# Optimization experiments

Hardware: AMD Instinct MI355X
Metric: run time of the kernel (lower is better)

Reference implementation:

```python
import jax, jax.numpy as jnp
import numpy as np

B, C, T, F = 4, 128, 512, 128
H, D = 4, 64              # n_head, hidden_channels
DV = C // H               # per-head value channels
EPS = 1e-5


def setup_inputs() -> dict:
    key = jax.random.key(0)
    ks = jax.random.split(key, 16)
    g = lambda k, s: jax.random.normal(k, s, dtype=jnp.float32) * 0.05
    inp = {
        'x': jax.random.normal(ks[0], (B, C, T, F), dtype=jnp.float32),
        # per-head Q/K/V 1x1 conv weights stacked over head axis
        'Wq': g(ks[1], (H, D, C)),  'bq': jnp.zeros((H, D), jnp.float32),
        'aq': jnp.full((H,), 0.25, jnp.float32),
        'lwq': jnp.ones((H, D, F), jnp.float32), 'lbq': jnp.zeros((H, D, F), jnp.float32),
        'Wk': g(ks[2], (H, D, C)),  'bk': jnp.zeros((H, D), jnp.float32),
        'ak': jnp.full((H,), 0.25, jnp.float32),
        'lwk': jnp.ones((H, D, F), jnp.float32), 'lbk': jnp.zeros((H, D, F), jnp.float32),
        'Wv': g(ks[3], (H, DV, C)), 'bv': jnp.zeros((H, DV), jnp.float32),
        'av': jnp.full((H,), 0.25, jnp.float32),
        'lwv': jnp.ones((H, DV, F), jnp.float32), 'lbv': jnp.zeros((H, DV, F), jnp.float32),
        # after_attention: 1x1 conv C->C + PReLU(scalar) + TLN([C, F])
        'Wo': g(ks[4], (C, C)), 'bo': jnp.zeros((C,), jnp.float32),
        'ao': jnp.float32(0.25),
        'lwo': jnp.ones((C, F), jnp.float32), 'lbo': jnp.zeros((C, F), jnp.float32),
    }
    return inp


def _proj(x, W, b, a, lw, lb):
    """1x1 conv (per head) + PReLU + LayerNorm over (channel, freq). x:[B,C,T,F] -> [B,H,D,T,F]."""
    y = jnp.einsum('bctf,hdc->bhdtf', x, W) + b[None, :, :, None, None]
    y = jnp.where(y >= 0, y, a[None, :, None, None, None] * y)
    mu = jnp.mean(y, axis=(2, 4), keepdims=True)
    var = jnp.mean(jnp.square(y - mu), axis=(2, 4), keepdims=True)
    y = (y - mu) * jax.lax.rsqrt(var + EPS)
    return y * lw[None, :, :, None, :] + lb[None, :, :, None, :]


def reference(x, Wq, bq, aq, lwq, lbq, Wk, bk, ak, lwk, lbk,
              Wv, bv, av, lwv, lbv, Wo, bo, ao, lwo, lbo):
    Bx, Cx, Tx, Fx = x.shape
    q = _proj(x, Wq, bq, aq, lwq, lbq)   # [B,H,D,T,F]
    k = _proj(x, Wk, bk, ak, lwk, lbk)   # [B,H,D,T,F]
    v = _proj(x, Wv, bv, av, lwv, lbv)   # [B,H,DV,T,F]
    # flatten as torch: transpose(1,2) then reshape -> feature layout (channel, freq)
    qf = q.transpose(0, 1, 3, 2, 4).reshape(Bx, H, Tx, D * Fx)
    kf = k.transpose(0, 1, 3, 2, 4).reshape(Bx, H, Tx, D * Fx)
    vf = v.transpose(0, 1, 3, 2, 4).reshape(Bx, H, Tx, DV * Fx)
    scale = 1.0 / jnp.sqrt(jnp.float32(Fx * D))
    attn = jax.nn.softmax(jnp.einsum('bhtd,bhsd->bhts', qf, kf) * scale, axis=-1)
    out = jnp.einsum('bhts,bhsd->bhtd', attn, vf)          # [B,H,T,DV*F]
    # concat heads (head-major) -> [B,T,C,F] -> [B,C,T,F]
    r = out.transpose(0, 2, 1, 3).reshape(Bx, Tx, Cx, Fx).transpose(0, 2, 1, 3)
    z = jnp.einsum('bctf,dc->bdtf', r, Wo) + bo[None, :, None, None]
    z = jnp.where(z >= 0, z, ao * z)
    mu = jnp.mean(z, axis=(1, 3), keepdims=True)
    var = jnp.mean(jnp.square(z - mu), axis=(1, 3), keepdims=True)
    z = (z - mu) * jax.lax.rsqrt(var + EPS)
    z = z * lwo[None, :, None, :] + lbo[None, :, None, :]
    return z + x
```

## Files before the change

kernel.cpp:

```cpp
#include <hip/hip_runtime.h>
#include <hip/hip_bf16.h>

constexpr int B = 4, C = 128, T = 512, F = 128, H = 4, D = 64, DV = 32;
constexpr int E  = D * F;
constexpr int EV = DV * F;
constexpr float EPS = 1e-5f;


typedef __attribute__((ext_vector_type(4))) float f32x4;
typedef __attribute__((ext_vector_type(8))) short bf16x8;

__device__ __forceinline__ float bf2f(unsigned short u) {
  return __uint_as_float(((unsigned int)u) << 16);
}
__device__ __forceinline__ unsigned short f2bf(float f) {
  unsigned int b = __float_as_uint(f);
  unsigned int r = b + 0x7FFFu + ((b >> 16) & 1u);
  return (unsigned short)(r >> 16);
}

__device__ __forceinline__ void gl_lds16(const unsigned short* g, unsigned short* l) {
  __builtin_amdgcn_global_load_lds(
      (const __attribute__((address_space(1))) unsigned int*)(g),
      (__attribute__((address_space(3))) unsigned int*)(l), 16, 0, 0);
}

__global__ __launch_bounds__(256) void prep_kernel(
    const float* __restrict__ Wq, const float* __restrict__ Wk,
    const float* __restrict__ Wv, const float* __restrict__ Wo,
    const float* __restrict__ bq, const float* __restrict__ bk,
    const float* __restrict__ bv, const float* __restrict__ aq,
    const float* __restrict__ ak, const float* __restrict__ av,
    const float* __restrict__ lwq, const float* __restrict__ lwk,
    const float* __restrict__ lwv, const float* __restrict__ lbq,
    const float* __restrict__ lbk, const float* __restrict__ lbv,
    unsigned short* __restrict__ Wall, unsigned short* __restrict__ Wo2,
    float* __restrict__ ball, float* __restrict__ aall,
    float* __restrict__ lwall, float* __restrict__ lball,
    float* __restrict__ lwI, float* __restrict__ lbI) {
  int i = blockIdx.x * 256 + threadIdx.x;
  if (i < 81920) {
    float w = (i < 32768) ? Wq[i] : (i < 65536) ? Wk[i - 32768] : Wv[i - 65536];
    Wall[i] = f2bf(w);
    float lw = (i < 32768) ? lwq[i] : (i < 65536) ? lwk[i - 32768] : lwv[i - 65536];
    float lb = (i < 32768) ? lbq[i] : (i < 65536) ? lbk[i - 32768] : lbv[i - 65536];
    lwall[i] = lw;
    lball[i] = lb;
    int gm = i >> 7, f = i & 127;
    if (gm >= 512) {
      int hm = gm - 512;
      size_t idx = ((size_t)(hm >> 2) * 128 + f) * 4 + (hm & 3);
      lwI[idx] = lw;
      lbI[idx] = lb;
    }
  }
  if (i < 16384) Wo2[i] = f2bf(Wo[i]);
  if (i < 640) {
    ball[i] = (i < 256) ? bq[i] : (i < 512) ? bk[i - 256] : bv[i - 512];
    aall[i] = (i < 256) ? aq[i >> 6] : (i < 512) ? ak[(i - 256) >> 6] : av[(i - 512) >> 5];
  }
}

__global__ __launch_bounds__(256) void xT_kernel(const float* __restrict__ x,
                                                 unsigned short* __restrict__ xT) {
  __shared__ unsigned short tile[128][136];
  int bx = blockIdx.x;
  int t = bx & 511;
  int b = bx >> 9;
  int tid = threadIdx.x;
#pragma unroll
  for (int j = 0; j < 16; ++j) {
    int ch = j * 256 + tid;
    int c = ch >> 5;
    int fc = ch & 31;
    float4 v = *reinterpret_cast<const float4*>(
        x + (((size_t)b * C + c) * T + t) * F + fc * 4);
    unsigned short o[4] = {f2bf(v.x), f2bf(v.y), f2bf(v.z), f2bf(v.w)};
    *reinterpret_cast<ushort4*>(&tile[c][fc * 4]) = *reinterpret_cast<const ushort4*>(o);
  }
  __syncthreads();
  int f = tid >> 1, half = tid & 1;
  unsigned short* dst = xT + ((size_t)b * 65536 + (size_t)t * 128 + f) * 128 + half * 64;
#pragma unroll
  for (int g8 = 0; g8 < 8; ++g8) {
    unsigned short o[8];
#pragma unroll
    for (int kk = 0; kk < 8; ++kk) o[kk] = tile[half * 64 + g8 * 8 + kk][f];
    *reinterpret_cast<uint4*>(dst + g8 * 8) = *reinterpret_cast<const uint4*>(o);
  }
}

__global__ __launch_bounds__(256) void proj_gemm_kernel(
    const unsigned short* __restrict__ Wall, const unsigned short* __restrict__ xT,
    const float* __restrict__ ball, const float* __restrict__ aall,
    const float* __restrict__ lwall, const float* __restrict__ lball,
    const float* __restrict__ lwI, const float* __restrict__ lbI,
    unsigned short* __restrict__ qf, unsigned short* __restrict__ kf,
    unsigned short* __restrict__ vf) {
  __shared__ alignas(16) unsigned short As[128 * 64];
  __shared__ alignas(16) unsigned short Bs[128 * 64];
  __shared__ float part[4][2][2];

  int p = blockIdx.x;
  int cpx = gridDim.x >> 3;
  int v = (p & 7) * cpx + (p >> 3);
  int bb = v / 2560;
  int tl = v - bb * 2560;
  int tm = tl / 512;
  int t = tl - tm * 512;

  int tid = threadIdx.x;
  int w = tid >> 6, lane = tid & 63;
  int wr = w >> 1, wc = w & 1;
  int lr = lane & 15, kg = lane >> 4;

  const unsigned short* Ab = Wall + (size_t)tm * 128 * 128;
  const unsigned short* Bb = xT + ((size_t)bb * 65536 + (size_t)t * 128) * 128;

  f32x4 acc[4][4] = {};
  for (int k0 = 0; k0 < 128; k0 += 64) {
#pragma unroll
    for (int j = 0; j < 4; ++j) {
      int ch = j * 256 + tid;
      int r = ch >> 3;
      int c = (ch & 7) * 8;
      gl_lds16(Ab + (size_t)r * 128 + k0 + c, &As[ch * 8]);
      gl_lds16(Bb + (size_t)r * 128 + k0 + c, &Bs[ch * 8]);
    }
    __syncthreads();
#pragma unroll
    for (int ks = 0; ks < 2; ++ks) {
      bf16x8 af[4], bfr[4];
#pragma unroll
      for (int m = 0; m < 4; ++m)
        af[m] = *reinterpret_cast<const bf16x8*>(
            &As[(wr * 64 + m * 16 + lr) * 64 + ks * 32 + kg * 8]);
#pragma unroll
      for (int n = 0; n < 4; ++n)
        bfr[n] = *reinterpret_cast<const bf16x8*>(
            &Bs[(wc * 64 + n * 16 + lr) * 64 + ks * 32 + kg * 8]);
#pragma unroll
      for (int m = 0; m < 4; ++m)
#pragma unroll
        for (int n = 0; n < 4; ++n)
          acc[m][n] = __builtin_amdgcn_mfma_f32_16x16x32_bf16(af[m], bfr[n], acc[m][n], 0, 0, 0);
    }
    __syncthreads();
  }

  int sec = (tm < 2) ? 0 : (tm < 4 ? 1 : 2);
  float s[2] = {0.f, 0.f}, s2[2] = {0.f, 0.f};
#pragma unroll
  for (int m = 0; m < 4; ++m) {
    int g = (sec == 2) ? (m >> 1) : 0;
    int gm0 = tm * 128 + wr * 64 + m * 16 + kg * 4;
    float4 bi4 = *reinterpret_cast<const float4*>(&ball[gm0]);
    float4 al4 = *reinterpret_cast<const float4*>(&aall[gm0]);
    const float bi[4] = {bi4.x, bi4.y, bi4.z, bi4.w};
    const float al[4] = {al4.x, al4.y, al4.z, al4.w};
#pragma unroll
    for (int j = 0; j < 4; ++j) {
#pragma unroll
      for (int n = 0; n < 4; ++n) {
        float val = acc[m][n][j] + bi[j];
        val = val >= 0.f ? val : al[j] * val;
        acc[m][n][j] = val;
        s[g] += val;
        s2[g] += val * val;
      }
    }
  }
#pragma unroll
  for (int off = 32; off >= 1; off >>= 1) {
    s[0] += __shfl_xor(s[0], off, 64);
    s2[0] += __shfl_xor(s2[0], off, 64);
    s[1] += __shfl_xor(s[1], off, 64);
    s2[1] += __shfl_xor(s2[1], off, 64);
  }
  if (lane == 0) {
    part[w][0][0] = s[0]; part[w][0][1] = s2[0];
    part[w][1][0] = s[1]; part[w][1][1] = s2[1];
  }
  __syncthreads();
  float invN = (sec == 2) ? (1.f / 4096.f) : (1.f / 8192.f);
  float mu[2], rs[2];
#pragma unroll
  for (int g = 0; g < 2; ++g) {
    float S = part[2 * wr][g][0] + part[2 * wr + 1][g][0];
    float S2 = part[2 * wr][g][1] + part[2 * wr + 1][g][1];
    float m_ = S * invN;
    float var = S2 * invN - m_ * m_;
    mu[g] = m_;
    rs[g] = rsqrtf(var + EPS);
  }

#pragma unroll
  for (int m = 0; m < 4; ++m) {
    int g = (sec == 2) ? (m >> 1) : 0;
    float mu_ = mu[g], rs_ = rs[g];
    int row0 = wr * 64 + m * 16 + kg * 4;
    int gm0 = tm * 128 + row0;
    if (sec < 2) {
#pragma unroll
      for (int j = 0; j < 4; ++j) {
        int gm = gm0 + j;
        const float* lwr = lwall + (size_t)gm * 128;
        const float* lbr = lball + (size_t)gm * 128;
        unsigned short* dst;
        if (sec == 0) {
          int h = gm >> 6, d = gm & 63;
          dst = qf + (((size_t)bb * H + h) * T + t) * E + d * 128;
        } else {
          int hm = gm - 256, h = hm >> 6, d = hm & 63;
          dst = kf + (((size_t)bb * H + h) * T + t) * E + d * 128;
        }
#pragma unroll
        for (int n = 0; n < 4; ++n) {
          int f = wc * 64 + n * 16 + lr;
          dst[f] = f2bf((acc[m][n][j] - mu_) * rs_ * lwr[f] + lbr[f]);
        }
      }
    } else {
      int hm = gm0 - 512;
      int h = hm >> 5, d0 = hm & 31;
      int gmg = hm >> 2;
      unsigned short* dstb = vf + (((size_t)bb * H + h) * T + t) * EV;
      const float* lw0 = lwI + (size_t)gmg * 512;
      const float* lb0 = lbI + (size_t)gmg * 512;
#pragma unroll
      for (int n = 0; n < 4; ++n) {
        int f = wc * 64 + n * 16 + lr;
        float4 w4 = *reinterpret_cast<const float4*>(lw0 + f * 4);
        float4 b4 = *reinterpret_cast<const float4*>(lb0 + f * 4);
        unsigned short o[4];
        o[0] = f2bf((acc[m][n][0] - mu_) * rs_ * w4.x + b4.x);
        o[1] = f2bf((acc[m][n][1] - mu_) * rs_ * w4.y + b4.y);
        o[2] = f2bf((acc[m][n][2] - mu_) * rs_ * w4.z + b4.z);
        o[3] = f2bf((acc[m][n][3] - mu_) * rs_ * w4.w + b4.w);
        *reinterpret_cast<ushort4*>(dstb + (size_t)f * 32 + d0) =
            *reinterpret_cast<const ushort4*>(o);
      }
    }
  }
}

template <bool OUT_BF16>
__global__ __launch_bounds__(256) void gemm_bt_kernel(
    const unsigned short* __restrict__ A, const unsigned short* __restrict__ Bm,
    void* __restrict__ Out, int M, int N, int K, float scale,
    int tiles_m, int tiles_n, int kchunks, int nb) {
  __shared__ alignas(16) unsigned short As[128 * 64];
  __shared__ alignas(16) unsigned short Bs[128 * 64];

  int p = blockIdx.x;
  int cpx = gridDim.x >> 3;
  int v = (p & 7) * cpx + (p >> 3);
  int tpb = tiles_m * tiles_n;
  int per_bh = tpb * kchunks;
  int bh = v / per_bh;
  int r0 = v - bh * per_bh;
  int kc = r0 / tpb;
  int tl = r0 - kc * tpb;
  int tm = tl / tiles_n;
  int tn = tl - tm * tiles_n;

  int tid = threadIdx.x;
  int w = tid >> 6, lane = tid & 63;
  int wr = w >> 1, wc = w & 1;
  int lr = lane & 15, kg = lane >> 4;

  const unsigned short* Ab = A + ((size_t)bh * M + tm * 128) * K;
  const unsigned short* Bb = Bm + ((size_t)bh * N + tn * 128) * K;

  int klen = K / kchunks;
  int kb = kc * klen;

  f32x4 acc[4][4] = {};
  for (int k0 = kb; k0 < kb + klen; k0 += 64) {
#pragma unroll
    for (int j = 0; j < 4; ++j) {
      int ch = j * 256 + tid;
      int r = ch >> 3;
      int c = (ch & 7) * 8;
      gl_lds16(Ab + (size_t)r * K + k0 + c, &As[ch * 8]);
      gl_lds16(Bb + (size_t)r * K + k0 + c, &Bs[ch * 8]);
    }
    __syncthreads();
#pragma unroll
    for (int ks = 0; ks < 2; ++ks) {
      bf16x8 af[4], bf[4];
#pragma unroll
      for (int m = 0; m < 4; ++m)
        af[m] = *reinterpret_cast<const bf16x8*>(
            &As[(wr * 64 + m * 16 + lr) * 64 + ks * 32 + kg * 8]);
#pragma unroll
      for (int n = 0; n < 4; ++n)
        bf[n] = *reinterpret_cast<const bf16x8*>(
            &Bs[(wc * 64 + n * 16 + lr) * 64 + ks * 32 + kg * 8]);
#pragma unroll
      for (int m = 0; m < 4; ++m)
#pragma unroll
        for (int n = 0; n < 4; ++n)
          acc[m][n] = __builtin_amdgcn_mfma_f32_16x16x32_bf16(af[m], bf[n], acc[m][n], 0, 0, 0);
    }
    __syncthreads();
  }

  int orow = tm * 128 + wr * 64 + kg * 4;
  int ocol = tn * 128 + wc * 64 + lr;
  size_t obase = (size_t)(kc * nb + bh) * M * N;
  if constexpr (OUT_BF16) {
    unsigned short* O = (unsigned short*)Out + obase;
#pragma unroll
    for (int m = 0; m < 4; ++m)
#pragma unroll
      for (int j = 0; j < 4; ++j) {
        size_t base = (size_t)(orow + m * 16 + j) * N + ocol;
#pragma unroll
        for (int n = 0; n < 4; ++n)
          O[base + n * 16] = f2bf(acc[m][n][j] * scale);
      }
  } else {
    float* O = (float*)Out + obase;
#pragma unroll
    for (int m = 0; m < 4; ++m)
#pragma unroll
      for (int j = 0; j < 4; ++j) {
        size_t base = (size_t)(orow + m * 16 + j) * N + ocol;
#pragma unroll
        for (int n = 0; n < 4; ++n)
          O[base + n * 16] = acc[m][n][j] * scale;
      }
  }
}

__global__ __launch_bounds__(256) void transpose_v_kernel(
    const unsigned short* __restrict__ src, unsigned short* __restrict__ dst) {
  __shared__ unsigned short tile[64][72];
  int bx = blockIdx.x;
  int et = bx & 63;
  int tt = (bx >> 6) & 7;
  int bh = bx >> 9;
  const unsigned short* sb = src + ((size_t)bh * T + tt * 64) * EV + et * 64;
#pragma unroll
  for (int j = 0; j < 2; ++j) {
    int ch = j * 256 + threadIdx.x;
    int r = ch >> 3;
    int c8 = ch & 7;
    uint4 u = *reinterpret_cast<const uint4*>(sb + (size_t)r * EV + c8 * 8);
    *reinterpret_cast<uint4*>(&tile[r][c8 * 8]) = u;
  }
  __syncthreads();
  unsigned short* db = dst + ((size_t)bh * EV + et * 64) * T + tt * 64;
#pragma unroll
  for (int j = 0; j < 2; ++j) {
    int ch = j * 256 + threadIdx.x;
    int r = ch >> 3;
    int c8 = ch & 7;
    unsigned short o[8];
#pragma unroll
    for (int i = 0; i < 8; ++i) o[i] = tile[c8 * 8 + i][r];
    *reinterpret_cast<uint4*>(db + (size_t)r * T + c8 * 8) =
        *reinterpret_cast<const uint4*>(o);
  }
}

__global__ __launch_bounds__(64) void softmax_kernel(const float* __restrict__ a,
                                                     unsigned short* __restrict__ ob,
                                                     int nchunk) {
  const size_t cs = (size_t)8192 * 512;
  const float* pr = a + (size_t)blockIdx.x * T;
  int tid = threadIdx.x;
  float4 v0 = *reinterpret_cast<const float4*>(pr + tid * 8);
  float4 v1 = *reinterpret_cast<const float4*>(pr + tid * 8 + 4);
  for (int c = 1; c < nchunk; ++c) {
    float4 u0 = *reinterpret_cast<const float4*>(pr + c * cs + tid * 8);
    float4 u1 = *reinterpret_cast<const float4*>(pr + c * cs + tid * 8 + 4);
    v0.x += u0.x; v0.y += u0.y; v0.z += u0.z; v0.w += u0.w;
    v1.x += u1.x; v1.y += u1.y; v1.z += u1.z; v1.w += u1.w;
  }
  float mx = fmaxf(fmaxf(fmaxf(v0.x, v0.y), fmaxf(v0.z, v0.w)),
                   fmaxf(fmaxf(v1.x, v1.y), fmaxf(v1.z, v1.w)));
#pragma unroll
  for (int off = 32; off >= 1; off >>= 1) mx = fmaxf(mx, __shfl_xor(mx, off, 64));
  v0.x = __expf(v0.x - mx); v0.y = __expf(v0.y - mx);
  v0.z = __expf(v0.z - mx); v0.w = __expf(v0.w - mx);
  v1.x = __expf(v1.x - mx); v1.y = __expf(v1.y - mx);
  v1.z = __expf(v1.z - mx); v1.w = __expf(v1.w - mx);
  float sm = v0.x + v0.y + v0.z + v0.w + v1.x + v1.y + v1.z + v1.w;
#pragma unroll
  for (int off = 32; off >= 1; off >>= 1) sm += __shfl_xor(sm, off, 64);
  float r = 1.0f / sm;
  uint4 o;
  o.x = (unsigned int)f2bf(v0.x * r) | ((unsigned int)f2bf(v0.y * r) << 16);
  o.y = (unsigned int)f2bf(v0.z * r) | ((unsigned int)f2bf(v0.w * r) << 16);
  o.z = (unsigned int)f2bf(v1.x * r) | ((unsigned int)f2bf(v1.y * r) << 16);
  o.w = (unsigned int)f2bf(v1.z * r) | ((unsigned int)f2bf(v1.w * r) << 16);
  *reinterpret_cast<uint4*>(ob + (size_t)blockIdx.x * T + tid * 8) = o;
}

__global__ __launch_bounds__(256) void outproj_gemm_kernel(
    const unsigned short* __restrict__ Wo2, const unsigned short* __restrict__ pv,
    const float* __restrict__ bo, const float* __restrict__ ao,
    const float* __restrict__ lwo, const float* __restrict__ lbo,
    const float* __restrict__ x, float* __restrict__ outp) {
  __shared__ alignas(16) unsigned short As[128 * 64];
  __shared__ alignas(16) unsigned short Bs[128 * 64];
  __shared__ float part[4][2];

  int p = blockIdx.x;
  int cpx = gridDim.x >> 3;
  int v = (p & 7) * cpx + (p >> 3);
  int bb = v >> 9;
  int t = v & 511;

  int tid = threadIdx.x;
  int w = tid >> 6, lane = tid & 63;
  int wr = w >> 1, wc = w & 1;
  int lr = lane & 15, kg = lane >> 4;

  const unsigned short* pvb = pv + (size_t)bb * H * T * EV + (size_t)t * EV;

  f32x4 acc[4][4] = {};
  for (int k0 = 0; k0 < 128; k0 += 64) {
#pragma unroll
    for (int j = 0; j < 4; ++j) {
      int ch = j * 256 + tid;
      int r = ch >> 3;
      int c0 = (ch & 7) * 8;
      gl_lds16(Wo2 + (size_t)r * 128 + k0 + c0, &As[ch * 8]);
      int cc = k0 + c0;
      int h = cc >> 5, dv0 = cc & 31;
      gl_lds16(pvb + (size_t)h * T * EV + (size_t)r * 32 + dv0, &Bs[ch * 8]);
    }
    __syncthreads();
#pragma unroll
    for (int ks = 0; ks < 2; ++ks) {
      bf16x8 af[4], bf[4];
#pragma unroll
      for (int m = 0; m < 4; ++m)
        af[m] = *reinterpret_cast<const bf16x8*>(
            &As[(wr * 64 + m * 16 + lr) * 64 + ks * 32 + kg * 8]);
#pragma unroll
      for (int n = 0; n < 4; ++n)
        bf[n] = *reinterpret_cast<const bf16x8*>(
            &Bs[(wc * 64 + n * 16 + lr) * 64 + ks * 32 + kg * 8]);
#pragma unroll
      for (int m = 0; m < 4; ++m)
#pragma unroll
        for (int n = 0; n < 4; ++n)
          acc[m][n] = __builtin_amdgcn_mfma_f32_16x16x32_bf16(af[m], bf[n], acc[m][n], 0, 0, 0);
    }
    __syncthreads();
  }

  float aO = ao[0];
  float s = 0.f, s2 = 0.f;
#pragma unroll
  for (int m = 0; m < 4; ++m)
#pragma unroll
    for (int j = 0; j < 4; ++j) {
      int d = wr * 64 + m * 16 + kg * 4 + j;
      float bi = bo[d];
#pragma unroll
      for (int n = 0; n < 4; ++n) {
        float val = acc[m][n][j] + bi;
        val = val >= 0.f ? val : aO * val;
        acc[m][n][j] = val;
        s += val;
        s2 += val * val;
      }
    }
#pragma unroll
  for (int off = 32; off >= 1; off >>= 1) {
    s += __shfl_xor(s, off, 64);
    s2 += __shfl_xor(s2, off, 64);
  }
  if (lane == 0) { part[w][0] = s; part[w][1] = s2; }
  __syncthreads();
  float S = part[0][0] + part[1][0] + part[2][0] + part[3][0];
  float S2 = part[0][1] + part[1][1] + part[2][1] + part[3][1];
  const float invN = 1.f / 16384.f;
  float mu = S * invN;
  float var = S2 * invN - mu * mu;
  float rstd = rsqrtf(var + EPS);
#pragma unroll
  for (int m = 0; m < 4; ++m)
#pragma unroll
    for (int j = 0; j < 4; ++j) {
      int d = wr * 64 + m * 16 + kg * 4 + j;
#pragma unroll
      for (int n = 0; n < 4; ++n) {
        int f = wc * 64 + n * 16 + lr;
        float val = (acc[m][n][j] - mu) * rstd * lwo[d * 128 + f] + lbo[d * 128 + f];
        size_t xi = (((size_t)bb * C + d) * T + t) * F + f;
        outp[xi] = val + x[xi];
      }
    }
}

extern "C" void kernel_launch(void* const* d_in, const int* in_sizes, int n_in,
                              void* d_out, int out_size, void* d_ws, size_t ws_size,
                              hipStream_t stream) {
  const float* x   = (const float*)d_in[0];
  const float* Wq  = (const float*)d_in[1];
  const float* bq  = (const float*)d_in[2];
  const float* aq  = (const float*)d_in[3];
  const float* lwq = (const float*)d_in[4];
  const float* lbq = (const float*)d_in[5];
  const float* Wk  = (const float*)d_in[6];
  const float* bk_ = (const float*)d_in[7];
  const float* ak  = (const float*)d_in[8];
  const float* lwk = (const float*)d_in[9];
  const float* lbk = (const float*)d_in[10];
  const float* Wv  = (const float*)d_in[11];
  const float* bv  = (const float*)d_in[12];
  const float* av  = (const float*)d_in[13];
  const float* lwv = (const float*)d_in[14];
  const float* lbv = (const float*)d_in[15];
  const float* Wo  = (const float*)d_in[16];
  const float* bo  = (const float*)d_in[17];
  const float* ao  = (const float*)d_in[18];
  const float* lwo = (const float*)d_in[19];
  const float* lbo = (const float*)d_in[20];
  float* outp = (float*)d_out;

  char* ws = (char*)d_ws;
  unsigned short* qfp = (unsigned short*)(ws);
  unsigned short* kfp = (unsigned short*)(ws + 134217728ull);
  unsigned short* vfp = (unsigned short*)(ws + 268435456ull);
  unsigned short* xT  = (unsigned short*)(ws + 335544320ull);
  float*          atnP = (float*)(ws + 335544320ull);
  unsigned short* Wall = (unsigned short*)(ws + 402653184ull);
  unsigned short* Wo2  = (unsigned short*)(ws + 402849792ull);
  float*          lwall = (float*)(ws + 402915328ull);
  float*          lball = (float*)(ws + 403243008ull);
  float*          ball = (float*)(ws + 403570688ull);
  float*          aall = (float*)(ws + 403574784ull);
  float*          lwI  = (float*)(ws + 403578880ull);
  float*          lbI  = (float*)(ws + 403644416ull);
  unsigned short* atnb = (unsigned short*)(ws);
  unsigned short* vfT  = (unsigned short*)(ws + 134217728ull);
  unsigned short* pvp  = (unsigned short*)(ws + 268435456ull);

  prep_kernel<<<320, 256, 0, stream>>>(Wq, Wk, Wv, Wo, bq, bk_, bv, aq, ak, av,
                                       lwq, lwk, lwv, lbq, lbk, lbv,
                                       Wall, Wo2, ball, aall, lwall, lball,
                                       lwI, lbI);

  xT_kernel<<<2048, 256, 0, stream>>>(x, xT);

  proj_gemm_kernel<<<10240, 256, 0, stream>>>(Wall, xT, ball, aall,
                                              lwall, lball, lwI, lbI,
                                              qfp, kfp, vfp);

  gemm_bt_kernel<false><<<1024, 256, 0, stream>>>(
      qfp, kfp, atnP, 512, 512, 8192, 0.011048543456039806f, 4, 4, 4, 16);

  transpose_v_kernel<<<8192, 256, 0, stream>>>(vfp, vfT);

  softmax_kernel<<<8192, 64, 0, stream>>>(atnP, atnb, 4);

  gemm_bt_kernel<true><<<2048, 256, 0, stream>>>(
      atnb, vfT, pvp, 512, 4096, 512, 1.0f, 4, 32, 1, 16);

  outproj_gemm_kernel<<<2048, 256, 0, stream>>>(Wo2, pvp, bo, ao, lwo, lbo, x, outp);
}
```

Baseline: 546.6 us.

## Store QK^T split-K partials in fp16, halve split count, reuse bf16 xT residual

The QK^T GEMM now uses 2 K-chunks instead of 4 and writes its partial scores as fp16 instead of fp32. The softmax kernel reads and sums these fp16 partials, which cuts the bytes written and read for the score partials. The output projection now takes its residual from the bf16 transposed copy xT, prefetched into LDS with a swizzle, instead of reading fp32 x from global memory. The risks are lower precision in the scores and in the residual add (bf16 x added to the output), fewer QK blocks for parallelism, and workspace offsets that were reshuffled so the partials fit in a new region.

```diff
diff --git a/kernel.cpp b/kernel.cpp
--- a/kernel.cpp
+++ b/kernel.cpp
@@ -1,5 +1,6 @@
 #include <hip/hip_runtime.h>
 #include <hip/hip_bf16.h>
+#include <hip/hip_fp16.h>
 
 constexpr int B = 4, C = 128, T = 512, F = 128, H = 4, D = 64, DV = 32;
 constexpr int E  = D * F;
@@ -17,6 +18,13 @@
   unsigned int b = __float_as_uint(f);
   unsigned int r = b + 0x7FFFu + ((b >> 16) & 1u);
   return (unsigned short)(r >> 16);
+}
+__device__ __forceinline__ unsigned short f2h(float f) {
+  __half h = __float2half(f);
+  return __half_as_ushort(h);
+}
+__device__ __forceinline__ float h2f(unsigned short u) {
+  return __half2float(__ushort_as_half(u));
 }
 
 __device__ __forceinline__ void gl_lds16(const unsigned short* g, unsigned short* l) {
@@ -244,7 +252,7 @@
   }
 }
 
-template <bool OUT_BF16>
+template <int OMODE>
 __global__ __launch_bounds__(256) void gemm_bt_kernel(
     const unsigned short* __restrict__ A, const unsigned short* __restrict__ Bm,
     void* __restrict__ Out, int M, int N, int K, float scale,
@@ -309,7 +317,7 @@
   int orow = tm * 128 + wr * 64 + kg * 4;
   int ocol = tn * 128 + wc * 64 + lr;
   size_t obase = (size_t)(kc * nb + bh) * M * N;
-  if constexpr (OUT_BF16) {
+  if constexpr (OMODE == 1) {
     unsigned short* O = (unsigned short*)Out + obase;
 #pragma unroll
     for (int m = 0; m < 4; ++m)
@@ -319,6 +327,17 @@
 #pragma unroll
         for (int n = 0; n < 4; ++n)
           O[base + n * 16] = f2bf(acc[m][n][j] * scale);
+      }
+  } else if constexpr (OMODE == 2) {
+    unsigned short* O = (unsigned short*)Out + obase;
+#pragma unroll
+    for (int m = 0; m < 4; ++m)
+#pragma unroll
+      for (int j = 0; j < 4; ++j) {
+        size_t base = (size_t)(orow + m * 16 + j) * N + ocol;
+#pragma unroll
+        for (int n = 0; n < 4; ++n)
+          O[base + n * 16] = f2h(acc[m][n][j] * scale);
       }
   } else {
     float* O = (float*)Out + obase;
@@ -365,47 +384,51 @@
   }
 }
 
-__global__ __launch_bounds__(64) void softmax_kernel(const float* __restrict__ a,
+__global__ __launch_bounds__(64) void softmax_kernel(const unsigned short* __restrict__ a,
                                                      unsigned short* __restrict__ ob,
                                                      int nchunk) {
   const size_t cs = (size_t)8192 * 512;
-  const float* pr = a + (size_t)blockIdx.x * T;
+  const unsigned short* pr = a + (size_t)blockIdx.x * T;
   int tid = threadIdx.x;
-  float4 v0 = *reinterpret_cast<const float4*>(pr + tid * 8);
-  float4 v1 = *reinterpret_cast<const float4*>(pr + tid * 8 + 4);
+  float v[8];
+  uint4 u = *reinterpret_cast<const uint4*>(pr + tid * 8);
+  const unsigned short* up = reinterpret_cast<const unsigned short*>(&u);
+#pragma unroll
+  for (int i = 0; i < 8; ++i) v[i] = h2f(up[i]);
   for (int c = 1; c < nchunk; ++c) {
-    float4 u0 = *reinterpret_cast<const float4*>(pr + c * cs + tid * 8);
-    float4 u1 = *reinterpret_cast<const float4*>(pr + c * cs + tid * 8 + 4);
-    v0.x += u0.x; v0.y += u0.y; v0.z += u0.z; v0.w += u0.w;
-    v1.x += u1.x; v1.y += u1.y; v1.z += u1.z; v1.w += u1.w;
-  }
-  float mx = fmaxf(fmaxf(fmaxf(v0.x, v0.y), fmaxf(v0.z, v0.w)),
-                   fmaxf(fmaxf(v1.x, v1.y), fmaxf(v1.z, v1.w)));
+    uint4 u2 = *reinterpret_cast<const uint4*>(pr + c * cs + tid * 8);
+    const unsigned short* u2p = reinterpret_cast<const unsigned short*>(&u2);
+#pragma unroll
+    for (int i = 0; i < 8; ++i) v[i] += h2f(u2p[i]);
+  }
+  float mx = v[0];
+#pragma unroll
+  for (int i = 1; i < 8; ++i) mx = fmaxf(mx, v[i]);
 #pragma unroll
   for (int off = 32; off >= 1; off >>= 1) mx = fmaxf(mx, __shfl_xor(mx, off, 64));
-  v0.x = __expf(v0.x - mx); v0.y = __expf(v0.y - mx);
-  v0.z = __expf(v0.z - mx); v0.w = __expf(v0.w - mx);
-  v1.x = __expf(v1.x - mx); v1.y = __expf(v1.y - mx);
-  v1.z = __expf(v1.z - mx); v1.w = __expf(v1.w - mx);
-  float sm = v0.x + v0.y + v0.z + v0.w + v1.x + v1.y + v1.z + v1.w;
+  float sm = 0.f;
+#pragma unroll
+  for (int i = 0; i < 8; ++i) { v[i] = __expf(v[i] - mx); sm += v[i]; }
 #pragma unroll
   for (int off = 32; off >= 1; off >>= 1) sm += __shfl_xor(sm, off, 64);
   float r = 1.0f / sm;
-  uint4 o;
-  o.x = (unsigned int)f2bf(v0.x * r) | ((unsigned int)f2bf(v0.y * r) << 16);
-  o.y = (unsigned int)f2bf(v0.z * r) | ((unsigned int)f2bf(v0.w * r) << 16);
-  o.z = (unsigned int)f2bf(v1.x * r) | ((unsigned int)f2bf(v1.y * r) << 16);
-  o.w = (unsigned int)f2bf(v1.z * r) | ((unsigned int)f2bf(v1.w * r) << 16);
-  *reinterpret_cast<uint4*>(ob + (size_t)blockIdx.x * T + tid * 8) = o;
+  unsigned short o[8];
+#pragma unroll
+  for (int i = 0; i < 8; ++i) o[i] = f2bf(v[i] * r);
+  *reinterpret_cast<uint4*>(ob + (size_t)blockIdx.x * T + tid * 8) =
+      *reinterpret_cast<const uint4*>(o);
 }
 
 __global__ __launch_bounds__(256) void outproj_gemm_kernel(
     const unsigned short* __restrict__ Wo2, const unsigned short* __restrict__ pv,
+    const unsigned short* __restrict__ xT,
     const float* __restrict__ bo, const float* __restrict__ ao,
     const float* __restrict__ lwo, const float* __restrict__ lbo,
-    const float* __restrict__ x, float* __restrict__ outp) {
-  __shared__ alignas(16) unsigned short As[128 * 64];
-  __shared__ alignas(16) unsigned short Bs[128 * 64];
+    float* __restrict__ outp) {
+  __shared__ alignas(16) unsigned short Sm[2 * 128 * 64];
+  unsigned short* As = Sm;
+  unsigned short* Bs = Sm + 128 * 64;
+  unsigned short* Rs = Sm;
   __shared__ float part[4][2];
 
   int p = blockIdx.x;
@@ -454,6 +477,15 @@
     __syncthreads();
   }
 
+  const unsigned short* xTb = xT + ((size_t)bb * 65536 + (size_t)t * 128) * 128;
+#pragma unroll
+  for (int j = 0; j < 8; ++j) {
+    int ch = j * 256 + tid;
+    int f = ch >> 4;
+    int s = ch & 15;
+    gl_lds16(xTb + (size_t)f * 128 + ((s ^ (f & 15)) * 8), &Rs[ch * 8]);
+  }
+
   float aO = ao[0];
   float s = 0.f, s2 = 0.f;
 #pragma unroll
@@ -485,18 +517,23 @@
   float var = S2 * invN - mu * mu;
   float rstd = rsqrtf(var + EPS);
 #pragma unroll
-  for (int m = 0; m < 4; ++m)
-#pragma unroll
-    for (int j = 0; j < 4; ++j) {
-      int d = wr * 64 + m * 16 + kg * 4 + j;
-#pragma unroll
-      for (int n = 0; n < 4; ++n) {
-        int f = wc * 64 + n * 16 + lr;
+  for (int m = 0; m < 4; ++m) {
+    int d0 = wr * 64 + m * 16 + kg * 4;
+#pragma unroll
+    for (int n = 0; n < 4; ++n) {
+      int f = wc * 64 + n * 16 + lr;
+      int ra = f * 128 + (((d0 >> 3) ^ (f & 15)) << 3) + (d0 & 7);
+      ushort4 rv = *reinterpret_cast<const ushort4*>(&Rs[ra]);
+      const unsigned short* rp = reinterpret_cast<const unsigned short*>(&rv);
+#pragma unroll
+      for (int j = 0; j < 4; ++j) {
+        int d = d0 + j;
         float val = (acc[m][n][j] - mu) * rstd * lwo[d * 128 + f] + lbo[d * 128 + f];
         size_t xi = (((size_t)bb * C + d) * T + t) * F + f;
-        outp[xi] = val + x[xi];
-      }
-    }
+        outp[xi] = val + bf2f(rp[j]);
+      }
+    }
+  }
 }
 
 extern "C" void kernel_launch(void* const* d_in, const int* in_sizes, int n_in,
@@ -530,15 +567,15 @@
   unsigned short* kfp = (unsigned short*)(ws + 134217728ull);
   unsigned short* vfp = (unsigned short*)(ws + 268435456ull);
   unsigned short* xT  = (unsigned short*)(ws + 335544320ull);
-  float*          atnP = (float*)(ws + 335544320ull);
-  unsigned short* Wall = (unsigned short*)(ws + 402653184ull);
-  unsigned short* Wo2  = (unsigned short*)(ws + 402849792ull);
-  float*          lwall = (float*)(ws + 402915328ull);
-  float*          lball = (float*)(ws + 403243008ull);
-  float*          ball = (float*)(ws + 403570688ull);
-  float*          aall = (float*)(ws + 403574784ull);
-  float*          lwI  = (float*)(ws + 403578880ull);
-  float*          lbI  = (float*)(ws + 403644416ull);
+  unsigned short* Wo2   = (unsigned short*)(ws + 402653184ull);
+  unsigned short* Wall  = (unsigned short*)(ws + 402685952ull);
+  float*          lwall = (float*)(ws + 402849792ull);
+  float*          lball = (float*)(ws + 403177472ull);
+  float*          ball  = (float*)(ws + 403505152ull);
+  float*          aall  = (float*)(ws + 403509248ull);
+  float*          lwI   = (float*)(ws + 403513344ull);
+  float*          lbI   = (float*)(ws + 403578880ull);
+  unsigned short* atnP = (unsigned short*)(ws + 402685952ull);
   unsigned short* atnb = (unsigned short*)(ws);
   unsigned short* vfT  = (unsigned short*)(ws + 134217728ull);
   unsigned short* pvp  = (unsigned short*)(ws + 268435456ull);
@@ -554,15 +591,15 @@
                                               lwall, lball, lwI, lbI,
                                               qfp, kfp, vfp);
 
-  gemm_bt_kernel<false><<<1024, 256, 0, stream>>>(
-      qfp, kfp, atnP, 512, 512, 8192, 0.011048543456039806f, 4, 4, 4, 16);
+  gemm_bt_kernel<2><<<512, 256, 0, stream>>>(
+      qfp, kfp, atnP, 512, 512, 8192, 0.011048543456039806f, 4, 4, 2, 16);
 
   transpose_v_kernel<<<8192, 256, 0, stream>>>(vfp, vfT);
 
-  softmax_kernel<<<8192, 64, 0, stream>>>(atnP, atnb, 4);
-
-  gemm_bt_kernel<true><<<2048, 256, 0, stream>>>(
+  softmax_kernel<<<8192, 64, 0, stream>>>(atnP, atnb, 2);
+
+  gemm_bt_kernel<1><<<2048, 256, 0, stream>>>(
       atnb, vfT, pvp, 512, 4096, 512, 1.0f, 4, 32, 1, 16);
 
-  outproj_gemm_kernel<<<2048, 256, 0, stream>>>(Wo2, pvp, bo, ao, lwo, lbo, x, outp);
-}
+  outproj_gemm_kernel<<<2048, 256, 0, stream>>>(Wo2, pvp, xT, bo, ao, lwo, lbo, outp);
+}
```

Result: faster. 500.8 us, median of 2 (-8.4%).
